# Performance work log

Hardware: AMD Instinct MI355X
Metric: run time of the kernel (lower is better)

The kernel has to match this reference:

```python
import jax, jax.numpy as jnp
import numpy as np

B, N, D, H, K, NH = 4096, 2048, 1024, 4096, 5, 8
HD = D // NH  # head dim


def setup_inputs() -> dict:
    key = jax.random.key(0)
    ks = jax.random.split(key, 12)
    s_d = np.float32(1.0 / np.sqrt(D))
    s_h = np.float32(1.0 / np.sqrt(H))
    rn = lambda k, sh, s: jax.random.normal(k, sh, dtype=jnp.float32) * s
    return {
        "morph0": jax.random.normal(ks[0], (B, D), dtype=jnp.float32),
        "stored_morph0": jax.random.normal(ks[1], (N, D), dtype=jnp.float32),
        "stored_morph1": jax.random.normal(ks[2], (N, D), dtype=jnp.float32),
        "wq": rn(ks[3], (D, D), s_d), "bq": jnp.zeros((D,), jnp.float32),
        "wk": rn(ks[4], (D, D), s_d), "bk": jnp.zeros((D,), jnp.float32),
        "wv": rn(ks[5], (D, D), s_d), "bv": jnp.zeros((D,), jnp.float32),
        "wo": rn(ks[6], (D, D), s_d), "bo": jnp.zeros((D,), jnp.float32),
        "w1": rn(ks[7], (H, D), s_d), "b1": jnp.zeros((H,), jnp.float32),
        "w2": rn(ks[8], (H, H), s_h), "b2": jnp.zeros((H,), jnp.float32),
        "w3": rn(ks[9], (D, H), s_h), "b3": jnp.zeros((D,), jnp.float32),
    }


def _l2norm(x):
    # F.normalize(dim=1): x / max(||x||, eps)
    n = jnp.sqrt(jnp.sum(x * x, axis=-1, keepdims=True))
    return x / jnp.maximum(n, 1e-12)


def reference(morph0, stored_morph0, stored_morph1,
              wq, bq, wk, bk, wv, bv, wo, bo,
              w1, b1, w2, b2, w3, b3):
    # ---- retrieve similar patterns: cosine sim + topk + fused gather-subtract ----
    qn = _l2norm(morph0)                       # [B, D]
    sn = _l2norm(stored_morph0)                # [N, D]
    sim = qn @ sn.T                            # [B, N]
    _, top_idx = jax.lax.top_k(sim, K)         # [B, K]
    evo = stored_morph1 - stored_morph0        # [N, D]
    selected = jnp.take(evo, top_idx, axis=0)  # [B, K, D] evolution vectors

    # ---- torch.nn.MultiheadAttention(D, 8, batch_first=True), eval mode ----
    q = (morph0 @ wq.T + bq).reshape(B, 1, NH, HD)      # [B, 1, NH, HD]
    k = (selected @ wk.T + bk).reshape(B, K, NH, HD)    # [B, K, NH, HD]
    v = (selected @ wv.T + bv).reshape(B, K, NH, HD)
    scores = jnp.einsum('bqhd,bkhd->bhqk', q, k) / np.float32(np.sqrt(HD))  # [B, NH, 1, K]
    attn = jax.nn.softmax(scores, axis=-1)
    ctx = jnp.einsum('bhqk,bkhd->bqhd', attn, v).reshape(B, 1, D)
    context = (ctx @ wo.T + bo)[:, 0, :]                # [B, D]
    attn_weights = attn.mean(axis=1)                    # [B, 1, K] (avg over heads)

    # ---- evolution net (dropout inactive in eval) + residual ----
    x = morph0 + context
    h1 = jax.nn.relu(x @ w1.T + b1)
    h2 = jax.nn.relu(h1 @ w2.T + b2)
    predicted = morph0 + (h2 @ w3.T + b3)
    return predicted, attn_weights
```

## Files before the change

### kernel.cpp

```cpp
#include <hip/hip_runtime.h>
#include <hip/hip_bf16.h>
#include <math.h>

typedef __bf16 bf16_t;
typedef __bf16 bf16x4 __attribute__((ext_vector_type(4)));
typedef __bf16 bf16x8 __attribute__((ext_vector_type(8)));
typedef float  f32x4  __attribute__((ext_vector_type(4)));

#define BB 4096
#define NN 2048
#define DD 1024
#define HH 4096
#define KSEL 5
#define NHEAD 8

__device__ __forceinline__ unsigned short bfbits(float f) {
  return __builtin_bit_cast(unsigned short, (bf16_t)f);
}

__device__ __forceinline__ void gload_lds16(const void* g, void* l) {
  __builtin_amdgcn_global_load_lds(
      (const __attribute__((address_space(1))) void*)g,
      (__attribute__((address_space(3))) void*)l, 16, 0, 0);
}

__global__ void f2b_k(const float4* __restrict__ in, ushort4* __restrict__ out, int n4) {
  int i = blockIdx.x * 256 + threadIdx.x;
  if (i >= n4) return;
  float4 x = in[i];
  ushort4 o;
  o.x = bfbits(x.x); o.y = bfbits(x.y); o.z = bfbits(x.z); o.w = bfbits(x.w);
  out[i] = o;
}

__global__ void evo_k(const float4* __restrict__ a, const float4* __restrict__ b,
                      ushort4* __restrict__ out, int n4) {
  int i = blockIdx.x * 256 + threadIdx.x;
  if (i >= n4) return;
  float4 x = a[i], y = b[i];
  ushort4 o;
  o.x = bfbits(y.x - x.x); o.y = bfbits(y.y - x.y);
  o.z = bfbits(y.z - x.z); o.w = bfbits(y.w - x.w);
  out[i] = o;
}

__global__ void rnormd_k(const float* __restrict__ s0, double* __restrict__ rnd) {
  __shared__ double red[256];
  int n = blockIdx.x, tid = threadIdx.x;
  const float4* row = (const float4*)(s0 + (size_t)n * DD);
  float4 x = row[tid];
  double ss = (double)x.x * x.x + (double)x.y * x.y + (double)x.z * x.z + (double)x.w * x.w;
  red[tid] = ss; __syncthreads();
  for (int s = 128; s > 0; s >>= 1) {
    if (tid < s) red[tid] += red[tid + s];
    __syncthreads();
  }
  if (tid == 0) rnd[n] = 1.0 / fmax(sqrt(red[0]), 1e-12);
}

template<bool RELU, bool RESID, bool OUTBF16>
__global__ void __launch_bounds__(256)
gemm_bt(const bf16_t* __restrict__ A, const bf16_t* __restrict__ Bw,
        const float* __restrict__ bias, const float* __restrict__ resid,
        float* __restrict__ outf, bf16_t* __restrict__ outb,
        int M, int Nn, int Kk)
{
  __shared__ alignas(16) bf16_t At[2][4096];
  __shared__ alignas(16) bf16_t Bt[2][4096];
  const int tid = threadIdx.x;
  const int wave = tid >> 6, lane = tid & 63;
  const int wm = wave >> 1, wn = wave & 1;
  const int bm = blockIdx.y << 7, bn = blockIdx.x << 7;

  const int srow  = (wave << 4) + (lane >> 2);
  const int scolb = (lane & 3) << 4;
  const char* pA0 = (const char*)A  + (size_t)(bm + srow) * Kk * 2 + scolb;
  const char* pA1 = (const char*)A  + (size_t)(bm + srow + 64) * Kk * 2 + scolb;
  const char* pB0 = (const char*)Bw + (size_t)(bn + srow) * Kk * 2 + scolb;
  const char* pB1 = (const char*)Bw + (size_t)(bn + srow + 64) * Kk * 2 + scolb;

  f32x4 zero = {0.f, 0.f, 0.f, 0.f};
  f32x4 acc[4][4];
  #pragma unroll
  for (int i = 0; i < 4; ++i)
    #pragma unroll
    for (int j = 0; j < 4; ++j) acc[i][j] = zero;

  const int fAoff = ((wm << 6) + (lane & 15)) * 32 + ((lane >> 4) << 3);
  const int fBoff = ((wn << 6) + (lane & 15)) * 32 + ((lane >> 4) << 3);

  const int nt = Kk >> 5;
  {
    char* lA = (char*)At[0] + (wave << 10);
    char* lB = (char*)Bt[0] + (wave << 10);
    gload_lds16(pA0, lA);
    gload_lds16(pA1, lA + 4096);
    gload_lds16(pB0, lB);
    gload_lds16(pB1, lB + 4096);
  }
  __syncthreads();

  for (int t = 0; t < nt; ++t) {
    const int cur = t & 1;
    if (t + 1 < nt) {
      size_t kb = (size_t)(t + 1) << 6;
      char* lA = (char*)At[cur ^ 1] + (wave << 10);
      char* lB = (char*)Bt[cur ^ 1] + (wave << 10);
      gload_lds16(pA0 + kb, lA);
      gload_lds16(pA1 + kb, lA + 4096);
      gload_lds16(pB0 + kb, lB);
      gload_lds16(pB1 + kb, lB + 4096);
    }
    bf16x8 av[4], bv[4];
    #pragma unroll
    for (int i = 0; i < 4; ++i) av[i] = *(const bf16x8*)(&At[cur][fAoff + i * 512]);
    #pragma unroll
    for (int j = 0; j < 4; ++j) bv[j] = *(const bf16x8*)(&Bt[cur][fBoff + j * 512]);
    #pragma unroll
    for (int i = 0; i < 4; ++i)
      #pragma unroll
      for (int j = 0; j < 4; ++j)
        acc[i][j] = __builtin_amdgcn_mfma_f32_16x16x32_bf16(av[i], bv[j], acc[i][j], 0, 0, 0);
    __syncthreads();
  }

  const int r0 = bm + (wm << 6) + ((lane >> 4) << 2);
  const int c0 = bn + (wn << 6) + (lane & 15);
  #pragma unroll
  for (int i = 0; i < 4; ++i) {
    #pragma unroll
    for (int j = 0; j < 4; ++j) {
      #pragma unroll
      for (int r = 0; r < 4; ++r) {
        int row = r0 + i * 16 + r;
        int col = c0 + j * 16;
        size_t o = (size_t)row * Nn + col;
        float v = acc[i][j][r];
        if (bias)  v += bias[col];
        if (RESID) v += resid[o];
        if (RELU)  v = fmaxf(v, 0.f);
        if (OUTBF16) outb[o] = (bf16_t)v;
        else         outf[o] = v;
      }
    }
  }
}

template<bool RELU>
__global__ void __launch_bounds__(512, 2)
gemm8p(const bf16_t* __restrict__ A, const bf16_t* __restrict__ Bw,
       const float* __restrict__ bias, bf16_t* __restrict__ outb,
       int Nn, int Kk, int nbx)
{
  __shared__ alignas(16) bf16_t As[2][16384];
  __shared__ alignas(16) bf16_t Bs[2][16384];
  const int tid  = threadIdx.x;
  const int lane = tid & 63, wv = tid >> 6;
  const int wm = wv >> 2, wn = wv & 3;
  const int ln15 = lane & 15, ln4 = lane >> 4;

  const int nwg = gridDim.x;
  const int q = nwg >> 3, r = nwg & 7;
  const int xcd = blockIdx.x & 7, loc = blockIdx.x >> 3;
  const int swz = (xcd < r ? xcd * (q + 1) : r * (q + 1) + (xcd - r) * q) + loc;
  const int bm = (swz / nbx) << 8;
  const int bn = (swz % nbx) << 8;

  const int NT = Kk >> 6;

  f32x4 acc[8][4];
  f32x4 zero = {0.f, 0.f, 0.f, 0.f};
  #pragma unroll
  for (int i = 0; i < 8; ++i)
    #pragma unroll
    for (int j = 0; j < 4; ++j) acc[i][j] = zero;

  auto stage = [&](const bf16_t* g, int grow0, bf16_t* lds, int kt) {
    #pragma unroll
    for (int e = 0; e < 4; ++e) {
      int row = e * 64 + wv * 8 + (lane >> 3);
      int slot = (lane & 7) ^ (row & 7);
      gload_lds16(g + (size_t)(grow0 + row) * Kk + kt * 64 + slot * 8,
                  (char*)lds + e * 8192 + wv * 1024);
    }
  };

  stage(A, bm, As[0], 0);
  stage(Bw, bn, Bs[0], 0);
  __syncthreads();

#define DS_A(MH)                                                                 \
    _Pragma("unroll") for (int mi = 0; mi < 4; ++mi)                             \
      _Pragma("unroll") for (int kk = 0; kk < 2; ++kk) {                         \
        const int row = wm * 128 + (MH) * 64 + mi * 16 + ln15;                   \
        const int slot = kk * 4 + ln4;                                           \
        av[mi][kk] = *(const bf16x8*)(Ab + row * 128 + ((slot ^ (row & 7)) << 4)); \
      }
#define DS_B(NH)                                                                 \
    _Pragma("unroll") for (int nj = 0; nj < 2; ++nj)                             \
      _Pragma("unroll") for (int kk = 0; kk < 2; ++kk) {                         \
        const int row = wn * 64 + (NH) * 32 + nj * 16 + ln15;                    \
        const int slot = kk * 4 + ln4;                                           \
        bv[nj][kk] = *(const bf16x8*)(Bb + row * 128 + ((slot ^ (row & 7)) << 4)); \
      }
#define MMA(MH, NH)                                                              \
    __builtin_amdgcn_s_setprio(1);                                               \
    _Pragma("unroll") for (int kk = 0; kk < 2; ++kk)                             \
      _Pragma("unroll") for (int mi = 0; mi < 4; ++mi)                           \
        _Pragma("unroll") for (int nj = 0; nj < 2; ++nj)                         \
          acc[(MH)*4+mi][(NH)*2+nj] = __builtin_amdgcn_mfma_f32_16x16x32_bf16(   \
              av[mi][kk], bv[nj][kk], acc[(MH)*4+mi][(NH)*2+nj], 0, 0, 0);       \
    __builtin_amdgcn_s_setprio(0);

  for (int t = 0; t < NT; ++t) {
    const int cur = t & 1;
    const char* Ab = (const char*)As[cur];
    const char* Bb = (const char*)Bs[cur];
    const bool more = (t + 1 < NT);
    bf16x8 av[4][2], bv[2][2];

    DS_A(0); DS_B(0);
    if (more) stage(A, bm, As[cur ^ 1], t + 1);
    __builtin_amdgcn_s_barrier();
    MMA(0, 0);
    __builtin_amdgcn_s_barrier();

    DS_A(1);
    if (more) stage(Bw, bn, Bs[cur ^ 1], t + 1);
    __builtin_amdgcn_s_barrier();
    MMA(1, 0);
    __builtin_amdgcn_s_barrier();

    DS_A(0); DS_B(1);
    __builtin_amdgcn_s_barrier();
    MMA(0, 1);
    __builtin_amdgcn_s_barrier();

    DS_A(1);
    asm volatile("s_waitcnt vmcnt(0)" ::: "memory");
    __builtin_amdgcn_sched_barrier(0);
    __builtin_amdgcn_s_barrier();
    MMA(1, 1);
    __builtin_amdgcn_s_barrier();
  }
#undef DS_A
#undef DS_B
#undef MMA

  #pragma unroll
  for (int am = 0; am < 8; ++am) {
    #pragma unroll
    for (int an = 0; an < 4; ++an) {
      #pragma unroll
      for (int rr = 0; rr < 4; ++rr) {
        int row = bm + wm * 128 + am * 16 + (lane >> 4) * 4 + rr;
        int col = bn + wn * 64 + an * 16 + ln15;
        float v = acc[am][an][rr] + bias[col];
        if (RELU) v = fmaxf(v, 0.f);
        outb[(size_t)row * Nn + col] = (bf16_t)v;
      }
    }
  }
}

__global__ void __launch_bounds__(256)
topk8_k(const float* __restrict__ sim, const double* __restrict__ rnd,
        int* __restrict__ cand)
{
  __shared__ float vals[NN];
  __shared__ float rv[256];
  __shared__ int   ri[256];
  int b = blockIdx.x, tid = threadIdx.x;
  for (int t = 0; t < NN / 256; ++t) {
    int i = tid + t * 256;
    vals[i] = sim[(size_t)b * NN + i] * (float)rnd[i];
  }
  __syncthreads();
  for (int p = 0; p < 8; ++p) {
    float bvv = -INFINITY; int bi = NN;
    for (int t = 0; t < NN / 256; ++t) {
      int i = tid + t * 256;
      float v = vals[i];
      if (v > bvv) { bvv = v; bi = i; }
    }
    rv[tid] = bvv; ri[tid] = bi;
    __syncthreads();
    for (int s = 128; s > 0; s >>= 1) {
      if (tid < s) {
        float v2 = rv[tid + s]; int i2 = ri[tid + s];
        if (v2 > rv[tid] || (v2 == rv[tid] && i2 < ri[tid])) { rv[tid] = v2; ri[tid] = i2; }
      }
      __syncthreads();
    }
    if (tid == 0) {
      int wsel = ri[0];
      cand[b * 8 + p] = wsel;
      vals[wsel] = -INFINITY;
    }
    __syncthreads();
  }
}

__global__ void __launch_bounds__(256)
refine_k(const float* __restrict__ m0, const float* __restrict__ s0,
         const double* __restrict__ rnd, const int* __restrict__ cand,
         int* __restrict__ topidx)
{
  __shared__ double red[256];
  __shared__ double vals[8];
  int b = blockIdx.x, tid = threadIdx.x;
  int cs[8];
  #pragma unroll
  for (int j = 0; j < 8; ++j) cs[j] = cand[b * 8 + j];
  const float* q = m0 + (size_t)b * DD;
  double part[8];
  #pragma unroll
  for (int j = 0; j < 8; ++j) part[j] = 0.0;
  for (int d = tid; d < DD; d += 256) {
    double qd = (double)q[d];
    #pragma unroll
    for (int j = 0; j < 8; ++j)
      part[j] += qd * (double)s0[(size_t)cs[j] * DD + d];
  }
  for (int j = 0; j < 8; ++j) {
    red[tid] = part[j]; __syncthreads();
    for (int s = 128; s > 0; s >>= 1) {
      if (tid < s) red[tid] += red[tid + s];
      __syncthreads();
    }
    if (tid == 0) vals[j] = red[0] * rnd[cs[j]];
    __syncthreads();
  }
  if (tid == 0) {
    bool used[8] = {false,false,false,false,false,false,false,false};
    for (int p = 0; p < KSEL; ++p) {
      int best = -1;
      for (int j = 0; j < 8; ++j) {
        if (used[j]) continue;
        if (best < 0 || vals[j] > vals[best] ||
            (vals[j] == vals[best] && cs[j] < cs[best])) best = j;
      }
      used[best] = true;
      topidx[b * KSEL + p] = cs[best];
    }
  }
}

__global__ void __launch_bounds__(256)
attn_k(const bf16_t* __restrict__ q, const bf16_t* __restrict__ eK,
       const bf16_t* __restrict__ eV, const int* __restrict__ tidx,
       bf16_t* __restrict__ ctx, float* __restrict__ attn_out)
{
  __shared__ float aw[NHEAD][KSEL];
  const int b = blockIdx.x, t = threadIdx.x;
  const int d0 = t << 2;
  int idx[KSEL];
  #pragma unroll
  for (int j = 0; j < KSEL; ++j) idx[j] = tidx[b * KSEL + j];

  bf16x4 qv = *(const bf16x4*)(q + (size_t)b * DD + d0);
  float s[KSEL];
  #pragma unroll
  for (int j = 0; j < KSEL; ++j) {
    bf16x4 kv = *(const bf16x4*)(eK + (size_t)idx[j] * DD + d0);
    float p = (float)qv[0] * (float)kv[0] + (float)qv[1] * (float)kv[1]
            + (float)qv[2] * (float)kv[2] + (float)qv[3] * (float)kv[3];
    #pragma unroll
    for (int m = 16; m > 0; m >>= 1) p += __shfl_xor(p, m);
    s[j] = p * 0.08838834764831845f;
  }
  float mx = s[0];
  #pragma unroll
  for (int j = 1; j < KSEL; ++j) mx = fmaxf(mx, s[j]);
  float e[KSEL], sum = 0.f;
  #pragma unroll
  for (int j = 0; j < KSEL; ++j) { e[j] = expf(s[j] - mx); sum += e[j]; }
  float inv = 1.f / sum;

  float c0 = 0.f, c1 = 0.f, c2 = 0.f, c3 = 0.f;
  #pragma unroll
  for (int j = 0; j < KSEL; ++j) {
    float a = e[j] * inv;
    bf16x4 vv = *(const bf16x4*)(eV + (size_t)idx[j] * DD + d0);
    c0 += a * (float)vv[0]; c1 += a * (float)vv[1];
    c2 += a * (float)vv[2]; c3 += a * (float)vv[3];
    if ((t & 31) == 0) aw[t >> 5][j] = a;
  }
  bf16x4 co; co[0] = (bf16_t)c0; co[1] = (bf16_t)c1; co[2] = (bf16_t)c2; co[3] = (bf16_t)c3;
  *(bf16x4*)(ctx + (size_t)b * DD + d0) = co;
  __syncthreads();
  if (t < KSEL) {
    float m = 0.f;
    #pragma unroll
    for (int hh = 0; hh < NHEAD; ++hh) m += aw[hh][t];
    attn_out[(size_t)b * KSEL + t] = m * 0.125f;
  }
}

extern "C" void kernel_launch(void* const* d_in, const int* in_sizes, int n_in,
                              void* d_out, int out_size, void* d_ws, size_t ws_size,
                              hipStream_t stream) {
  (void)in_sizes; (void)n_in; (void)out_size; (void)ws_size;
  const float* morph0 = (const float*)d_in[0];
  const float* s0     = (const float*)d_in[1];
  const float* s1     = (const float*)d_in[2];
  const float* wq = (const float*)d_in[3];  const float* bq = (const float*)d_in[4];
  const float* wk = (const float*)d_in[5];  const float* bk = (const float*)d_in[6];
  const float* wv = (const float*)d_in[7];  const float* bv = (const float*)d_in[8];
  const float* wo = (const float*)d_in[9];  const float* bo = (const float*)d_in[10];
  const float* w1 = (const float*)d_in[11]; const float* b1 = (const float*)d_in[12];
  const float* w2 = (const float*)d_in[13]; const float* b2 = (const float*)d_in[14];
  const float* w3 = (const float*)d_in[15]; const float* b3 = (const float*)d_in[16];

  char* ws = (char*)d_ws;
  size_t off = 0;
  auto alloc = [&](size_t bytes) { char* p = ws + off; off += (bytes + 255) & ~(size_t)255; return p; };

  float*  sim  = (float*) alloc((size_t)BB * NN * 4);
  bf16_t* m0b  = (bf16_t*)alloc((size_t)BB * DD * 2);
  bf16_t* s0b  = (bf16_t*)alloc((size_t)NN * DD * 2);
  bf16_t* evo  = (bf16_t*)alloc((size_t)NN * DD * 2);
  double* rnd  = (double*)alloc((size_t)NN * 8);
  int*    cand = (int*)   alloc((size_t)BB * 8 * 4);
  int*    tidx = (int*)   alloc((size_t)BB * KSEL * 4);
  bf16_t* qb   = (bf16_t*)alloc((size_t)BB * DD * 2);
  bf16_t* eKb  = (bf16_t*)alloc((size_t)NN * DD * 2);
  bf16_t* eVb  = (bf16_t*)alloc((size_t)NN * DD * 2);
  bf16_t* ctxb = (bf16_t*)alloc((size_t)BB * DD * 2);
  bf16_t* xb   = (bf16_t*)alloc((size_t)BB * DD * 2);
  bf16_t* wqb  = (bf16_t*)alloc((size_t)DD * DD * 2);
  bf16_t* wkb  = (bf16_t*)alloc((size_t)DD * DD * 2);
  bf16_t* wvb  = (bf16_t*)alloc((size_t)DD * DD * 2);
  bf16_t* wob  = (bf16_t*)alloc((size_t)DD * DD * 2);
  bf16_t* w1b  = (bf16_t*)alloc((size_t)HH * DD * 2);
  bf16_t* w2b  = (bf16_t*)alloc((size_t)HH * HH * 2);
  bf16_t* w3b  = (bf16_t*)alloc((size_t)DD * HH * 2);
  bf16_t* h2b  = (bf16_t*)alloc((size_t)BB * HH * 2);
  bf16_t* h1b  = (bf16_t*)sim;
  float*  attn_out = (float*)d_out + (size_t)BB * DD;

  auto f2b = [&](const float* in, bf16_t* out, size_t n) {
    f2b_k<<<dim3((unsigned)(n / 1024)), dim3(256), 0, stream>>>(
        (const float4*)in, (ushort4*)out, (int)(n / 4));
  };

  f2b(morph0, m0b, (size_t)BB * DD);
  f2b(s0,     s0b, (size_t)NN * DD);
  evo_k<<<dim3((NN * DD) / 1024), dim3(256), 0, stream>>>(
      (const float4*)s0, (const float4*)s1, (ushort4*)evo, (NN * DD) / 4);
  f2b(wq, wqb, (size_t)DD * DD);
  f2b(wk, wkb, (size_t)DD * DD);
  f2b(wv, wvb, (size_t)DD * DD);
  f2b(wo, wob, (size_t)DD * DD);
  f2b(w1, w1b, (size_t)HH * DD);
  f2b(w2, w2b, (size_t)HH * HH);
  f2b(w3, w3b, (size_t)DD * HH);
  rnormd_k<<<dim3(NN), dim3(256), 0, stream>>>(s0, rnd);

  gemm_bt<false,false,false><<<dim3(NN/128, BB/128), dim3(256), 0, stream>>>(
      m0b, s0b, nullptr, nullptr, sim, nullptr, BB, NN, DD);
  topk8_k<<<dim3(BB), dim3(256), 0, stream>>>(sim, rnd, cand);
  refine_k<<<dim3(BB), dim3(256), 0, stream>>>(morph0, s0, rnd, cand, tidx);

  gemm_bt<false,false,true><<<dim3(DD/128, BB/128), dim3(256), 0, stream>>>(
      m0b, wqb, bq, nullptr, nullptr, qb, BB, DD, DD);
  gemm_bt<false,false,true><<<dim3(DD/128, NN/128), dim3(256), 0, stream>>>(
      evo, wkb, bk, nullptr, nullptr, eKb, NN, DD, DD);
  gemm_bt<false,false,true><<<dim3(DD/128, NN/128), dim3(256), 0, stream>>>(
      evo, wvb, bv, nullptr, nullptr, eVb, NN, DD, DD);

  attn_k<<<dim3(BB), dim3(256), 0, stream>>>(qb, eKb, eVb, tidx, ctxb, attn_out);

  gemm_bt<false,true,true><<<dim3(DD/128, BB/128), dim3(256), 0, stream>>>(
      ctxb, wob, bo, morph0, nullptr, xb, BB, DD, DD);

  gemm8p<true><<<dim3((BB/256)*(HH/256)), dim3(512), 0, stream>>>(
      xb, w1b, b1, h1b, HH, DD, HH/256);
  gemm8p<true><<<dim3((BB/256)*(HH/256)), dim3(512), 0, stream>>>(
      h1b, w2b, b2, h2b, HH, HH, HH/256);
  gemm_bt<false,true,false><<<dim3(DD/128, BB/128), dim3(256), 0, stream>>>(
      h2b, w3b, b3, morph0, (float*)d_out, nullptr, BB, DD, HH);
}
```

Measured before the change: 562.9 us.

## Fuse fp32-to-bf16 prep kernels and split GEMM staging into finer-grained async loads

Replaces ten separate conversion/evo launches with one grid-stride prep kernel that converts all inputs and weights to bf16 in a single launch. In the 256x256 GEMM, global-to-LDS staging of the next k-tile is split into four quarter-loads spread across the four MMA phases, with partial vmcnt(4) waits instead of one full drain at the end. This aims to cut launch overhead and smooth memory traffic against MFMA work. The partial-wait accounting is delicate and could race or stall if the outstanding-load counts do not line up.

```diff
diff --git a/kernel.cpp b/kernel.cpp
--- a/kernel.cpp
+++ b/kernel.cpp
@@ -24,24 +24,63 @@
       (__attribute__((address_space(3))) void*)l, 16, 0, 0);
 }
 
-__global__ void f2b_k(const float4* __restrict__ in, ushort4* __restrict__ out, int n4) {
-  int i = blockIdx.x * 256 + threadIdx.x;
-  if (i >= n4) return;
-  float4 x = in[i];
+__device__ __forceinline__ ushort4 cvt4(float4 x) {
   ushort4 o;
   o.x = bfbits(x.x); o.y = bfbits(x.y); o.z = bfbits(x.z); o.w = bfbits(x.w);
-  out[i] = o;
-}
-
-__global__ void evo_k(const float4* __restrict__ a, const float4* __restrict__ b,
-                      ushort4* __restrict__ out, int n4) {
-  int i = blockIdx.x * 256 + threadIdx.x;
-  if (i >= n4) return;
-  float4 x = a[i], y = b[i];
-  ushort4 o;
-  o.x = bfbits(y.x - x.x); o.y = bfbits(y.y - x.y);
-  o.z = bfbits(y.z - x.z); o.w = bfbits(y.w - x.w);
-  out[i] = o;
+  return o;
+}
+
+#define P_M0   1048576
+#define P_S0   1572864
+#define P_EVO  2097152
+#define P_WQ   2359296
+#define P_WK   2621440
+#define P_WV   2883584
+#define P_WO   3145728
+#define P_W1   4194304
+#define P_W2   8388608
+#define P_W3   9437184
+__global__ void __launch_bounds__(256)
+prep_k(const float4* __restrict__ m0, const float4* __restrict__ s0,
+       const float4* __restrict__ s1,
+       const float4* __restrict__ wq, const float4* __restrict__ wk,
+       const float4* __restrict__ wv, const float4* __restrict__ wo,
+       const float4* __restrict__ w1, const float4* __restrict__ w2,
+       const float4* __restrict__ w3,
+       ushort4* __restrict__ m0b, ushort4* __restrict__ s0b,
+       ushort4* __restrict__ evo,
+       ushort4* __restrict__ wqb, ushort4* __restrict__ wkb,
+       ushort4* __restrict__ wvb, ushort4* __restrict__ wob,
+       ushort4* __restrict__ w1b, ushort4* __restrict__ w2b,
+       ushort4* __restrict__ w3b)
+{
+  const int stride = gridDim.x * 256;
+  for (int i = blockIdx.x * 256 + threadIdx.x; i < P_W3; i += stride) {
+    if (i < P_M0) {
+      m0b[i] = cvt4(m0[i]);
+    } else if (i < P_S0) {
+      int j = i - P_M0; s0b[j] = cvt4(s0[j]);
+    } else if (i < P_EVO) {
+      int j = i - P_S0;
+      float4 a = s0[j], b = s1[j];
+      float4 d; d.x = b.x - a.x; d.y = b.y - a.y; d.z = b.z - a.z; d.w = b.w - a.w;
+      evo[j] = cvt4(d);
+    } else if (i < P_WQ) {
+      int j = i - P_EVO; wqb[j] = cvt4(wq[j]);
+    } else if (i < P_WK) {
+      int j = i - P_WQ; wkb[j] = cvt4(wk[j]);
+    } else if (i < P_WV) {
+      int j = i - P_WK; wvb[j] = cvt4(wv[j]);
+    } else if (i < P_WO) {
+      int j = i - P_WV; wob[j] = cvt4(wo[j]);
+    } else if (i < P_W1) {
+      int j = i - P_WO; w1b[j] = cvt4(w1[j]);
+    } else if (i < P_W2) {
+      int j = i - P_W1; w2b[j] = cvt4(w2[j]);
+    } else {
+      int j = i - P_W2; w3b[j] = cvt4(w3[j]);
+    }
+  }
 }
 
 __global__ void rnormd_k(const float* __restrict__ s0, double* __restrict__ rnd) {
@@ -175,19 +214,31 @@
     #pragma unroll
     for (int j = 0; j < 4; ++j) acc[i][j] = zero;
 
-  auto stage = [&](const bf16_t* g, int grow0, bf16_t* lds, int kt) {
-    #pragma unroll
-    for (int e = 0; e < 4; ++e) {
-      int row = e * 64 + wv * 8 + (lane >> 3);
+  auto stageA = [&](int MH, bf16_t* lds, int kt) {
+    #pragma unroll
+    for (int u = 0; u < 2; ++u) {
+      int rowbase = u * 128 + MH * 64 + wv * 8;
+      int row = rowbase + (lane >> 3);
       int slot = (lane & 7) ^ (row & 7);
-      gload_lds16(g + (size_t)(grow0 + row) * Kk + kt * 64 + slot * 8,
-                  (char*)lds + e * 8192 + wv * 1024);
+      gload_lds16(A + (size_t)(bm + row) * Kk + kt * 64 + slot * 8,
+                  (char*)lds + rowbase * 128);
     }
   };
-
-  stage(A, bm, As[0], 0);
-  stage(Bw, bn, Bs[0], 0);
-  __syncthreads();
+  auto stageB = [&](int NH, bf16_t* lds, int kt) {
+    #pragma unroll
+    for (int u = 0; u < 2; ++u) {
+      int rowbase = u * 128 + ((wv >> 2) << 6) + NH * 32 + ((wv & 3) << 3);
+      int row = rowbase + (lane >> 3);
+      int slot = (lane & 7) ^ (row & 7);
+      gload_lds16(Bw + (size_t)(bn + row) * Kk + kt * 64 + slot * 8,
+                  (char*)lds + rowbase * 128);
+    }
+  };
+
+  stageA(0, As[0], 0); stageA(1, As[0], 0);
+  stageB(0, Bs[0], 0); stageB(1, Bs[0], 0);
+  asm volatile("s_waitcnt vmcnt(0)" ::: "memory");
+  __builtin_amdgcn_s_barrier();
 
 #define DS_A(MH)                                                                 \
     _Pragma("unroll") for (int mi = 0; mi < 4; ++mi)                             \
@@ -211,41 +262,50 @@
           acc[(MH)*4+mi][(NH)*2+nj] = __builtin_amdgcn_mfma_f32_16x16x32_bf16(   \
               av[mi][kk], bv[nj][kk], acc[(MH)*4+mi][(NH)*2+nj], 0, 0, 0);       \
     __builtin_amdgcn_s_setprio(0);
+#define VMW4                                                                     \
+    asm volatile("s_waitcnt vmcnt(4)" ::: "memory");                             \
+    __builtin_amdgcn_sched_barrier(0);
 
   for (int t = 0; t < NT; ++t) {
     const int cur = t & 1;
     const char* Ab = (const char*)As[cur];
     const char* Bb = (const char*)Bs[cur];
+    bf16_t* nA = As[cur ^ 1];
+    bf16_t* nB = Bs[cur ^ 1];
     const bool more = (t + 1 < NT);
     bf16x8 av[4][2], bv[2][2];
 
     DS_A(0); DS_B(0);
-    if (more) stage(A, bm, As[cur ^ 1], t + 1);
+    if (more) stageA(0, nA, t + 1);
     __builtin_amdgcn_s_barrier();
     MMA(0, 0);
+    VMW4;
     __builtin_amdgcn_s_barrier();
 
     DS_A(1);
-    if (more) stage(Bw, bn, Bs[cur ^ 1], t + 1);
+    if (more) stageB(0, nB, t + 1);
     __builtin_amdgcn_s_barrier();
     MMA(1, 0);
+    VMW4;
     __builtin_amdgcn_s_barrier();
 
     DS_A(0); DS_B(1);
+    if (more) stageA(1, nA, t + 1);
     __builtin_amdgcn_s_barrier();
     MMA(0, 1);
     __builtin_amdgcn_s_barrier();
 
     DS_A(1);
-    asm volatile("s_waitcnt vmcnt(0)" ::: "memory");
-    __builtin_amdgcn_sched_barrier(0);
+    if (more) stageB(1, nB, t + 1);
     __builtin_amdgcn_s_barrier();
     MMA(1, 1);
+    VMW4;
     __builtin_amdgcn_s_barrier();
   }
 #undef DS_A
 #undef DS_B
 #undef MMA
+#undef VMW4
 
   #pragma unroll
   for (int am = 0; am < 8; ++am) {
@@ -439,22 +499,13 @@
   bf16_t* h1b  = (bf16_t*)sim;
   float*  attn_out = (float*)d_out + (size_t)BB * DD;
 
-  auto f2b = [&](const float* in, bf16_t* out, size_t n) {
-    f2b_k<<<dim3((unsigned)(n / 1024)), dim3(256), 0, stream>>>(
-        (const float4*)in, (ushort4*)out, (int)(n / 4));
-  };
-
-  f2b(morph0, m0b, (size_t)BB * DD);
-  f2b(s0,     s0b, (size_t)NN * DD);
-  evo_k<<<dim3((NN * DD) / 1024), dim3(256), 0, stream>>>(
-      (const float4*)s0, (const float4*)s1, (ushort4*)evo, (NN * DD) / 4);
-  f2b(wq, wqb, (size_t)DD * DD);
-  f2b(wk, wkb, (size_t)DD * DD);
-  f2b(wv, wvb, (size_t)DD * DD);
-  f2b(wo, wob, (size_t)DD * DD);
-  f2b(w1, w1b, (size_t)HH * DD);
-  f2b(w2, w2b, (size_t)HH * HH);
-  f2b(w3, w3b, (size_t)DD * HH);
+  prep_k<<<dim3(2048), dim3(256), 0, stream>>>(
+      (const float4*)morph0, (const float4*)s0, (const float4*)s1,
+      (const float4*)wq, (const float4*)wk, (const float4*)wv, (const float4*)wo,
+      (const float4*)w1, (const float4*)w2, (const float4*)w3,
+      (ushort4*)m0b, (ushort4*)s0b, (ushort4*)evo,
+      (ushort4*)wqb, (ushort4*)wkb, (ushort4*)wvb, (ushort4*)wob,
+      (ushort4*)w1b, (ushort4*)w2b, (ushort4*)w3b);
   rnormd_k<<<dim3(NN), dim3(256), 0, stream>>>(s0, rnd);
 
   gemm_bt<false,false,false><<<dim3(NN/128, BB/128), dim3(256), 0, stream>>>(
```

New measurement: 549.2 us. 2.4% less time.
